# Kernel tuning notes

Measured on AMD Instinct MI355X. Metric: run time of the kernel, lower is better.

## Reference

```python
import jax, jax.numpy as jnp
import numpy as np


def setup_inputs() -> dict:
    key = jax.random.key(0)
    k1, k2 = jax.random.split(key)
    NUM_INS, NUM_CLASS = 8192, 5000
    # probabilities strictly inside (0,1) so log terms are finite
    output = jax.random.uniform(k1, (NUM_INS, NUM_CLASS), dtype=jnp.float32,
                                minval=1e-6, maxval=1.0 - 1e-6)
    # labels in {0,1,2}; 2 == ignore
    target = jax.random.randint(k2, (NUM_INS, NUM_CLASS), 0, 3, dtype=jnp.int64)
    return {"output": output, "target": target}


def reference(output, target):
    is_pos = target == 1
    is_neg = target == 0
    # masked BCE: -log(p) for positives, -log(1-p) for negatives, 0 where target==2
    per_elem = jnp.where(is_pos, -jnp.log(output),
                         jnp.where(is_neg, -jnp.log1p(-output), 0.0))
    count = jnp.sum(is_pos | is_neg)
    cost = jnp.sum(per_elem) / count.astype(per_elem.dtype)
    return cost
```

## Files before the change

kernel.cpp:

```cpp
#include <hip/hip_runtime.h>


__global__ __launch_bounds__(256) void bce_reduce_kernel(
    const float* __restrict__ prob,
    const int* __restrict__ tgt,
    float* __restrict__ ws_sum,
    unsigned int* __restrict__ ws_cnt,
    long long n4, long long n)
{
    const long long tid    = (long long)blockIdx.x * blockDim.x + threadIdx.x;
    const long long stride = (long long)gridDim.x * blockDim.x;

    float        lsum = 0.0f;
    unsigned int lcnt = 0u;

    const float4* __restrict__ p4 = (const float4*)prob;
    const int4*   __restrict__ t4 = (const int4*)tgt;

    for (long long i = tid; i < n4; i += stride) {
        float4 p = p4[i];
        int4   t = t4[i];

        {
            float v = (t.x == 1) ? p.x : 1.0f - p.x;
            float l = -logf(v);
            bool  c = (unsigned)t.x <= 1u;
            lsum += c ? l : 0.0f;
            lcnt += c ? 1u : 0u;
        }
        {
            float v = (t.y == 1) ? p.y : 1.0f - p.y;
            float l = -logf(v);
            bool  c = (unsigned)t.y <= 1u;
            lsum += c ? l : 0.0f;
            lcnt += c ? 1u : 0u;
        }
        {
            float v = (t.z == 1) ? p.z : 1.0f - p.z;
            float l = -logf(v);
            bool  c = (unsigned)t.z <= 1u;
            lsum += c ? l : 0.0f;
            lcnt += c ? 1u : 0u;
        }
        {
            float v = (t.w == 1) ? p.w : 1.0f - p.w;
            float l = -logf(v);
            bool  c = (unsigned)t.w <= 1u;
            lsum += c ? l : 0.0f;
            lcnt += c ? 1u : 0u;
        }
    }

    for (long long i = n4 * 4 + tid; i < n; i += stride) {
        float p = prob[i];
        int   t = tgt[i];
        float v = (t == 1) ? p : 1.0f - p;
        float l = -logf(v);
        bool  c = (unsigned)t <= 1u;
        lsum += c ? l : 0.0f;
        lcnt += c ? 1u : 0u;
    }

    #pragma unroll
    for (int off = 32; off > 0; off >>= 1) {
        lsum += __shfl_down(lsum, off, 64);
        lcnt += __shfl_down(lcnt, off, 64);
    }

    __shared__ float        s_sum[4];
    __shared__ unsigned int s_cnt[4];
    const int lane = threadIdx.x & 63;
    const int wave = threadIdx.x >> 6;
    if (lane == 0) {
        s_sum[wave] = lsum;
        s_cnt[wave] = lcnt;
    }
    __syncthreads();
    if (threadIdx.x == 0) {
        float        bsum = s_sum[0] + s_sum[1] + s_sum[2] + s_sum[3];
        unsigned int bcnt = s_cnt[0] + s_cnt[1] + s_cnt[2] + s_cnt[3];
        atomicAdd(ws_sum, bsum);
        atomicAdd(ws_cnt, bcnt);
    }
}

__global__ void bce_finalize_kernel(const float* __restrict__ ws_sum,
                                    const unsigned int* __restrict__ ws_cnt,
                                    float* __restrict__ out)
{
    out[0] = ws_sum[0] / (float)ws_cnt[0];
}

extern "C" void kernel_launch(void* const* d_in, const int* in_sizes, int n_in,
                              void* d_out, int out_size, void* d_ws, size_t ws_size,
                              hipStream_t stream) {
    const float* prob = (const float*)d_in[0];
    const int*   tgt  = (const int*)d_in[1];
    float*       out  = (float*)d_out;

    const long long n  = (long long)in_sizes[0];
    const long long n4 = n / 4;

    float*        ws_sum = (float*)d_ws;
    unsigned int* ws_cnt = (unsigned int*)((char*)d_ws + sizeof(float));

    hipMemsetAsync(d_ws, 0, sizeof(float) + sizeof(unsigned int), stream);

    const int block = 256;
    const int grid  = 2048;

    bce_reduce_kernel<<<grid, block, 0, stream>>>(prob, tgt, ws_sum, ws_cnt, n4, n);
    bce_finalize_kernel<<<1, 1, 0, stream>>>(ws_sum, ws_cnt, out);
}
```

Baseline: 357.0 us.

## Drop memset and atomics, unroll two float4 loads, use fast log

The reduce kernel now processes two float4/int4 pairs per iteration from the two halves of the array, which gives more loads in flight per thread. It uses the fast __logf intrinsic and 32-bit indexing. Each block writes its partial sum and count to its own workspace slot instead of doing global atomics, and a 256-thread finalize kernel reduces those slots, so the hipMemsetAsync is no longer needed. The risks are reduced accuracy from __logf and that the hardcoded grid size must match the workspace layout.

```diff
diff --git a/kernel.cpp b/kernel.cpp
--- a/kernel.cpp
+++ b/kernel.cpp
@@ -1,15 +1,21 @@
 #include <hip/hip_runtime.h>
 
 
-__global__ __launch_bounds__(256) void bce_reduce_kernel(
+#define GRID_BLOCKS 2048
+#define BLOCK 256
+
+__global__ __launch_bounds__(BLOCK) void bce_reduce_kernel(
     const float* __restrict__ prob,
     const int* __restrict__ tgt,
-    float* __restrict__ ws_sum,
-    unsigned int* __restrict__ ws_cnt,
-    long long n4, long long n)
+    float* __restrict__ part_sum,
+    unsigned int* __restrict__ part_cnt,
+    int n)
 {
-    const long long tid    = (long long)blockIdx.x * blockDim.x + threadIdx.x;
-    const long long stride = (long long)gridDim.x * blockDim.x;
+    const int tid    = blockIdx.x * BLOCK + threadIdx.x;
+    const int stride = GRID_BLOCKS * BLOCK;
+
+    const int n4  = n >> 2;
+    const int n4h = n4 >> 1;
 
     float        lsum = 0.0f;
     unsigned int lcnt = 0u;
@@ -17,46 +23,30 @@
     const float4* __restrict__ p4 = (const float4*)prob;
     const int4*   __restrict__ t4 = (const int4*)tgt;
 
-    for (long long i = tid; i < n4; i += stride) {
-        float4 p = p4[i];
-        int4   t = t4[i];
+    for (int i = tid; i < n4h; i += stride) {
+        float4 pa = p4[i];
+        int4   ta = t4[i];
+        float4 pb = p4[i + n4h];
+        int4   tb = t4[i + n4h];
 
-        {
-            float v = (t.x == 1) ? p.x : 1.0f - p.x;
-            float l = -logf(v);
-            bool  c = (unsigned)t.x <= 1u;
-            lsum += c ? l : 0.0f;
-            lcnt += c ? 1u : 0u;
+        #define ACC(P, T)                                   \
+        {                                                   \
+            float v = ((T) == 1) ? (P) : 1.0f - (P);        \
+            bool  c = (unsigned)(T) <= 1u;                  \
+            float l = -__logf(v);                           \
+            lsum += c ? l : 0.0f;                           \
+            lcnt += c ? 1u : 0u;                            \
         }
-        {
-            float v = (t.y == 1) ? p.y : 1.0f - p.y;
-            float l = -logf(v);
-            bool  c = (unsigned)t.y <= 1u;
-            lsum += c ? l : 0.0f;
-            lcnt += c ? 1u : 0u;
-        }
-        {
-            float v = (t.z == 1) ? p.z : 1.0f - p.z;
-            float l = -logf(v);
-            bool  c = (unsigned)t.z <= 1u;
-            lsum += c ? l : 0.0f;
-            lcnt += c ? 1u : 0u;
-        }
-        {
-            float v = (t.w == 1) ? p.w : 1.0f - p.w;
-            float l = -logf(v);
-            bool  c = (unsigned)t.w <= 1u;
-            lsum += c ? l : 0.0f;
-            lcnt += c ? 1u : 0u;
-        }
+        ACC(pa.x, ta.x) ACC(pa.y, ta.y) ACC(pa.z, ta.z) ACC(pa.w, ta.w)
+        ACC(pb.x, tb.x) ACC(pb.y, tb.y) ACC(pb.z, tb.z) ACC(pb.w, tb.w)
     }
 
-    for (long long i = n4 * 4 + tid; i < n; i += stride) {
+    for (int i = (n4h * 2) * 4 + tid; i < n; i += stride) {
         float p = prob[i];
         int   t = tgt[i];
         float v = (t == 1) ? p : 1.0f - p;
-        float l = -logf(v);
         bool  c = (unsigned)t <= 1u;
+        float l = -__logf(v);
         lsum += c ? l : 0.0f;
         lcnt += c ? 1u : 0u;
     }
@@ -71,24 +61,41 @@
     __shared__ unsigned int s_cnt[4];
     const int lane = threadIdx.x & 63;
     const int wave = threadIdx.x >> 6;
-    if (lane == 0) {
-        s_sum[wave] = lsum;
-        s_cnt[wave] = lcnt;
+    if (lane == 0) { s_sum[wave] = lsum; s_cnt[wave] = lcnt; }
+    __syncthreads();
+    if (threadIdx.x == 0) {
+        part_sum[blockIdx.x] = s_sum[0] + s_sum[1] + s_sum[2] + s_sum[3];
+        part_cnt[blockIdx.x] = s_cnt[0] + s_cnt[1] + s_cnt[2] + s_cnt[3];
     }
+}
+
+__global__ __launch_bounds__(BLOCK) void bce_finalize_kernel(
+    const float* __restrict__ part_sum,
+    const unsigned int* __restrict__ part_cnt,
+    float* __restrict__ out)
+{
+    float        lsum = 0.0f;
+    unsigned int lcnt = 0u;
+    for (int i = threadIdx.x; i < GRID_BLOCKS; i += BLOCK) {
+        lsum += part_sum[i];
+        lcnt += part_cnt[i];
+    }
+    #pragma unroll
+    for (int off = 32; off > 0; off >>= 1) {
+        lsum += __shfl_down(lsum, off, 64);
+        lcnt += __shfl_down(lcnt, off, 64);
+    }
+    __shared__ float        s_sum[4];
+    __shared__ unsigned int s_cnt[4];
+    const int lane = threadIdx.x & 63;
+    const int wave = threadIdx.x >> 6;
+    if (lane == 0) { s_sum[wave] = lsum; s_cnt[wave] = lcnt; }
     __syncthreads();
     if (threadIdx.x == 0) {
         float        bsum = s_sum[0] + s_sum[1] + s_sum[2] + s_sum[3];
         unsigned int bcnt = s_cnt[0] + s_cnt[1] + s_cnt[2] + s_cnt[3];
-        atomicAdd(ws_sum, bsum);
-        atomicAdd(ws_cnt, bcnt);
+        out[0] = bsum / (float)bcnt;
     }
-}
-
-__global__ void bce_finalize_kernel(const float* __restrict__ ws_sum,
-                                    const unsigned int* __restrict__ ws_cnt,
-                                    float* __restrict__ out)
-{
-    out[0] = ws_sum[0] / (float)ws_cnt[0];
 }
 
 extern "C" void kernel_launch(void* const* d_in, const int* in_sizes, int n_in,
@@ -98,17 +105,11 @@
     const int*   tgt  = (const int*)d_in[1];
     float*       out  = (float*)d_out;
 
-    const long long n  = (long long)in_sizes[0];
-    const long long n4 = n / 4;
+    const int n = in_sizes[0];
 
-    float*        ws_sum = (float*)d_ws;
-    unsigned int* ws_cnt = (unsigned int*)((char*)d_ws + sizeof(float));
+    float*        part_sum = (float*)d_ws;
+    unsigned int* part_cnt = (unsigned int*)((char*)d_ws + GRID_BLOCKS * sizeof(float));
 
-    hipMemsetAsync(d_ws, 0, sizeof(float) + sizeof(unsigned int), stream);
-
-    const int block = 256;
-    const int grid  = 2048;
-
-    bce_reduce_kernel<<<grid, block, 0, stream>>>(prob, tgt, ws_sum, ws_cnt, n4, n);
-    bce_finalize_kernel<<<1, 1, 0, stream>>>(ws_sum, ws_cnt, out);
+    bce_reduce_kernel<<<GRID_BLOCKS, BLOCK, 0, stream>>>(prob, tgt, part_sum, part_cnt, n);
+    bce_finalize_kernel<<<1, BLOCK, 0, stream>>>(part_sum, part_cnt, out);
 }
```

Result: faster. 329.7 us (-7.7%).
